# Kernel tuning notes

Hardware: AMD Instinct MI355X
Metric: run time of the kernel (lower is better)

## Reference

```python
import jax, jax.numpy as jnp
import numpy as np

B, SQ, SK, H, NH = 2, 2048, 2048, 1024, 16
HD = H // NH  # 64


def setup_inputs() -> dict:
    key = jax.random.key(0)
    ks = jax.random.split(key, 12)
    s = 1.0 / np.sqrt(H)
    inp = {
        "query": jax.random.normal(ks[0], (B, SQ, H), jnp.float32),
        "key": jax.random.normal(ks[1], (B, SK, H), jnp.float32),
        "value": jax.random.normal(ks[2], (B, SK, H), jnp.float32),
        # lower-triangular causal mask [B, SQ, SK]; nonzero = attend
        "causal_mask": jnp.broadcast_to(
            jnp.tril(jnp.ones((SQ, SK), jnp.int32)), (B, SQ, SK)
        ),
        "Wq": jax.random.uniform(ks[3], (H, H), jnp.float32, -s, s),
        "bq": jnp.zeros((H,), jnp.float32),
        "Wk": jax.random.uniform(ks[4], (H, H), jnp.float32, -s, s),
        "bk": jnp.zeros((H,), jnp.float32),
        "Wv": jax.random.uniform(ks[5], (H, H), jnp.float32, -s, s),
        "bv": jnp.zeros((H,), jnp.float32),
        "Wo": jax.random.uniform(ks[6], (H, H), jnp.float32, -s, s),
        "bo": jnp.zeros((H,), jnp.float32),
        "ln_g": jnp.ones((H,), jnp.float32),
        "ln_b": jnp.zeros((H,), jnp.float32),
    }
    return inp


def _layer_norm(x, g, b, eps=1e-5):
    mu = jnp.mean(x, axis=-1, keepdims=True)
    var = jnp.var(x, axis=-1, keepdims=True)
    return (x - mu) * jax.lax.rsqrt(var + eps) * g + b


def reference(query, key, value, causal_mask, Wq, bq, Wk, bk, Wv, bv, Wo, bo, ln_g, ln_b):
    # projections (torch Linear: x @ W.T + b)
    q = (query @ Wq.T + bq).reshape(B, SQ, NH, HD)
    k = (key @ Wk.T + bk).reshape(B, SK, NH, HD)
    v = (value @ Wv.T + bv).reshape(B, SK, NH, HD)
    # scores [B, NH, SQ, SK]
    scores = jnp.einsum("bqhd,bkhd->bhqk", q, k) / np.sqrt(HD).astype(np.float32)
    scores = jnp.where(causal_mask[:, None, :, :] == 0, -jnp.inf, scores)
    attn = jax.nn.softmax(scores, axis=-1)
    # dropout is identity in eval mode
    out = jnp.einsum("bhqk,bkhd->bqhd", attn, v).reshape(B, SQ, H)
    out = out @ Wo.T + bo
    return _layer_norm(query + out, ln_g, ln_b)
```

## Files before the change

### kernel.cpp

```cpp
#include <hip/hip_runtime.h>
#include <hip/hip_bf16.h>

#define SQL 2048
#define SKL 2048
#define HH  1024
#define NHH 16
#define HDD 64
#define BB  2
#define MM  (BB*SQL)

typedef __attribute__((ext_vector_type(8))) short short8;
typedef __attribute__((ext_vector_type(4))) short short4v;
typedef __attribute__((ext_vector_type(4))) float f32x4;
typedef unsigned short u16;

__device__ inline u16 f2bf(float f) {
    unsigned int u = __float_as_uint(f);
    u += 0x7fffu + ((u >> 16) & 1u);
    return (u16)(u >> 16);
}

__device__ inline void gl_lds16(const void* g, void* l) {
    __builtin_amdgcn_global_load_lds(
        (const __attribute__((address_space(1))) unsigned int*)g,
        (__attribute__((address_space(3))) unsigned int*)l, 16, 0, 0);
}

__global__ __launch_bounds__(256) void cvt_all_kernel(
    const float* __restrict__ q, const float* __restrict__ k, const float* __restrict__ v,
    const float* __restrict__ wq, const float* __restrict__ wk,
    const float* __restrict__ wv, const float* __restrict__ wo,
    u16* __restrict__ xq, u16* __restrict__ xk, u16* __restrict__ xv,
    u16* __restrict__ wqb, u16* __restrict__ wkb, u16* __restrict__ wvb, u16* __restrict__ wob)
{
    int b = blockIdx.x;
    const float* src; u16* dst;
    if      (b < 4096)  { src = q;  dst = xq; }
    else if (b < 8192)  { src = k;  dst = xk;  b -= 4096; }
    else if (b < 12288) { src = v;  dst = xv;  b -= 8192; }
    else if (b < 13312) { src = wq; dst = wqb; b -= 12288; }
    else if (b < 14336) { src = wk; dst = wkb; b -= 13312; }
    else if (b < 15360) { src = wv; dst = wvb; b -= 14336; }
    else                { src = wo; dst = wob; b -= 15360; }
    int i = (b * 256 + threadIdx.x) * 4;
    float4 vv = *(const float4*)(src + i);
    ushort4 oo;
    oo.x = f2bf(vv.x); oo.y = f2bf(vv.y); oo.z = f2bf(vv.z); oo.w = f2bf(vv.w);
    *(ushort4*)(dst + i) = oo;
}

__global__ __launch_bounds__(256) void proj_kernel(
    const u16* __restrict__ xq, const u16* __restrict__ xk, const u16* __restrict__ xv,
    const u16* __restrict__ wqb, const u16* __restrict__ wkb, const u16* __restrict__ wvb,
    const float* __restrict__ bq, const float* __restrict__ bk, const float* __restrict__ bv,
    u16* __restrict__ oq, u16* __restrict__ ok, u16* __restrict__ ov)
{
    const int z = blockIdx.z;
    const u16* A      = (z == 0) ? xq  : (z == 1) ? xk  : xv;
    const u16* W      = (z == 0) ? wqb : (z == 1) ? wkb : wvb;
    const float* bias = (z == 0) ? bq  : (z == 1) ? bk  : bv;
    u16* outb         = (z == 0) ? oq  : (z == 1) ? ok  : ov;
    const float scale = (z == 0) ? 0.125f * 1.4426950408889634f : 1.0f;

    __shared__ u16 lds_a[128 * 64];
    __shared__ u16 lds_b[128 * 64];

    const int t = threadIdx.x;
    const int lane = t & 63;
    const int quad = lane >> 4;
    const int lo = lane & 15;
    const int wv = t >> 6;
    const int wm = (wv >> 1) * 64, wn = (wv & 1) * 64;
    const int m0 = blockIdx.x * 128;
    const int n0 = blockIdx.y * 128;

    f32x4 acc[4][4];
#pragma unroll
    for (int i = 0; i < 4; i++)
#pragma unroll
        for (int j = 0; j < 4; j++) acc[i][j] = (f32x4){0.f, 0.f, 0.f, 0.f};

    int rr[4], cc[4];
#pragma unroll
    for (int u = 0; u < 4; u++) {
        int sl = u * 256 + t;
        rr[u] = sl >> 3;
        cc[u] = ((sl & 7) ^ (rr[u] & 7)) * 8;
    }

    for (int k0 = 0; k0 < HH; k0 += 64) {
#pragma unroll
        for (int u = 0; u < 4; u++) {
            gl_lds16(A + (size_t)(m0 + rr[u]) * HH + k0 + cc[u], &lds_a[(u * 256 + t) * 8]);
            gl_lds16(W + (size_t)(n0 + rr[u]) * HH + k0 + cc[u], &lds_b[(u * 256 + t) * 8]);
        }
        __syncthreads();
#pragma unroll
        for (int kk = 0; kk < 2; kk++) {
            short8 af[4], bf[4];
#pragma unroll
            for (int i = 0; i < 4; i++) {
                const int ra = wm + i * 16 + lo;
                const int rb = wn + i * 16 + lo;
                af[i] = *(const short8*)&lds_a[ra * 64 + (((kk * 4 + quad) ^ (ra & 7)) * 8)];
                bf[i] = *(const short8*)&lds_b[rb * 64 + (((kk * 4 + quad) ^ (rb & 7)) * 8)];
            }
            if (z == 2) {
#pragma unroll
                for (int i = 0; i < 4; i++)
#pragma unroll
                    for (int j = 0; j < 4; j++)
                        acc[i][j] = __builtin_amdgcn_mfma_f32_16x16x32_bf16(bf[j], af[i], acc[i][j], 0, 0, 0);
            } else {
#pragma unroll
                for (int i = 0; i < 4; i++)
#pragma unroll
                    for (int j = 0; j < 4; j++)
                        acc[i][j] = __builtin_amdgcn_mfma_f32_16x16x32_bf16(af[i], bf[j], acc[i][j], 0, 0, 0);
            }
        }
        __syncthreads();
    }

#pragma unroll
    for (int i = 0; i < 4; i++) {
#pragma unroll
        for (int j = 0; j < 4; j++) {
#pragma unroll
            for (int r = 0; r < 4; r++) {
                if (z == 2) {
                    int dg  = n0 + wn + j * 16 + quad * 4 + r;
                    int tok = m0 + wm + i * 16 + lo;
                    float val = acc[i][j][r] + bias[dg];
                    int head = dg >> 6, d = dg & 63;
                    int bi = tok >> 11, s = tok & 2047;
                    outb[(((size_t)bi * NHH + head) * HDD + d) * SKL + s] = f2bf(val);
                } else {
                    int row = m0 + wm + i * 16 + quad * 4 + r;
                    int col = n0 + wn + j * 16 + lo;
                    float val = (acc[i][j][r] + bias[col]) * scale;
                    int bi = row >> 11, s = row & 2047;
                    int head = col >> 6, d = col & 63;
                    outb[(((size_t)bi * NHH + head) * SQL + s) * HDD + d] = f2bf(val);
                }
            }
        }
    }
}

__global__ __launch_bounds__(256) void outproj_kernel(
    const u16* __restrict__ A, const u16* __restrict__ W,
    const float* __restrict__ bias, const float* __restrict__ resid,
    float* __restrict__ outf)
{
    __shared__ u16 lds_a[128 * 64];
    __shared__ u16 lds_b[128 * 64];

    const int t = threadIdx.x;
    const int lane = t & 63;
    const int quad = lane >> 4;
    const int lo = lane & 15;
    const int wv = t >> 6;
    const int wm = (wv >> 1) * 64, wn = (wv & 1) * 64;
    const int m0 = blockIdx.x * 128;
    const int n0 = blockIdx.y * 128;

    f32x4 acc[4][4];
#pragma unroll
    for (int i = 0; i < 4; i++)
#pragma unroll
        for (int j = 0; j < 4; j++) acc[i][j] = (f32x4){0.f, 0.f, 0.f, 0.f};

    int rr[4], cc[4];
#pragma unroll
    for (int u = 0; u < 4; u++) {
        int sl = u * 256 + t;
        rr[u] = sl >> 3;
        cc[u] = ((sl & 7) ^ (rr[u] & 7)) * 8;
    }

    for (int k0 = 0; k0 < HH; k0 += 64) {
#pragma unroll
        for (int u = 0; u < 4; u++) {
            gl_lds16(A + (size_t)(m0 + rr[u]) * HH + k0 + cc[u], &lds_a[(u * 256 + t) * 8]);
            gl_lds16(W + (size_t)(n0 + rr[u]) * HH + k0 + cc[u], &lds_b[(u * 256 + t) * 8]);
        }
        __syncthreads();
#pragma unroll
        for (int kk = 0; kk < 2; kk++) {
            short8 af[4], bf[4];
#pragma unroll
            for (int i = 0; i < 4; i++) {
                const int ra = wm + i * 16 + lo;
                const int rb = wn + i * 16 + lo;
                af[i] = *(const short8*)&lds_a[ra * 64 + (((kk * 4 + quad) ^ (ra & 7)) * 8)];
                bf[i] = *(const short8*)&lds_b[rb * 64 + (((kk * 4 + quad) ^ (rb & 7)) * 8)];
            }
#pragma unroll
            for (int i = 0; i < 4; i++)
#pragma unroll
                for (int j = 0; j < 4; j++)
                    acc[i][j] = __builtin_amdgcn_mfma_f32_16x16x32_bf16(af[i], bf[j], acc[i][j], 0, 0, 0);
        }
        __syncthreads();
    }

#pragma unroll
    for (int i = 0; i < 4; i++)
#pragma unroll
        for (int j = 0; j < 4; j++)
#pragma unroll
            for (int r = 0; r < 4; r++) {
                int row = m0 + wm + i * 16 + quad * 4 + r;
                int col = n0 + wn + j * 16 + lo;
                float val = acc[i][j][r] + bias[col] + resid[(size_t)row * HH + col];
                outf[(size_t)row * HH + col] = val;
            }
}

#define PSTR 72
#define KVB 128

__global__ __launch_bounds__(256) void attn_kernel(
    const u16* __restrict__ qb, const u16* __restrict__ kb, const u16* __restrict__ vtb,
    u16* __restrict__ attn_out)
{
    __shared__ u16 k_lds[KVB * 64];
    __shared__ u16 vt_lds[64 * KVB];
    __shared__ u16 p_lds[4 * 16 * PSTR];

    const int t = threadIdx.x;
    const int lane = t & 63;
    const int quad = lane >> 4;
    const int lo = lane & 15;
    const int w = t >> 6;
    const int qt = (SQL / 64 - 1) - (blockIdx.x >> 5);
    const int bh = blockIdx.x & 31;
    const int q0 = qt * 64;

    const u16* qbase = qb + ((size_t)bh * SQL + q0 + w * 16 + lo) * HDD + quad * 8;
    short8 qf0 = *(const short8*)qbase;
    short8 qf1 = *(const short8*)(qbase + 32);

    float m_s = -__builtin_inff(), l_s = 0.f;
    f32x4 o[4];
#pragma unroll
    for (int j = 0; j < 4; j++) o[j] = (f32x4){0.f, 0.f, 0.f, 0.f};

    int krr[4], kcc[4], vrr[4], vcc[4];
#pragma unroll
    for (int u = 0; u < 4; u++) {
        int sl = u * 256 + t;
        krr[u] = sl >> 3;  kcc[u] = ((sl & 7)  ^ (krr[u] & 7))  * 8;
        vrr[u] = sl >> 4;  vcc[u] = ((sl & 15) ^ (vrr[u] & 15)) * 8;
    }
    const u16* kbh = kb + (size_t)bh * SKL * HDD;
    const u16* vbh = vtb + (size_t)bh * HDD * SKL;
    u16* ppriv = &p_lds[w * 16 * PSTR];
    const int ql = w * 16 + lo;
    const int KT = (qt >> 1) + 1;

    for (int ti = 0; ti < KT; ti++) {
        const int k0 = ti * KVB;
#pragma unroll
        for (int u = 0; u < 4; u++) {
            gl_lds16(kbh + (size_t)(k0 + krr[u]) * HDD + kcc[u], &k_lds[(u * 256 + t) * 8]);
            gl_lds16(vbh + (size_t)vrr[u] * SKL + k0 + vcc[u], &vt_lds[(u * 256 + t) * 8]);
        }
        __syncthreads();

#pragma unroll
        for (int hb = 0; hb < 2; hb++) {
            const int kb0 = k0 + hb * 64;
            if (kb0 > q0) break;
            const bool diag = (kb0 == q0);

            f32x4 s[4];
            __builtin_amdgcn_s_setprio(1);
#pragma unroll
            for (int nt = 0; nt < 4; nt++) {
                const int row = hb * 64 + nt * 16 + lo;
                short8 kf0 = *(const short8*)&k_lds[row * 64 + ((quad ^ (row & 7)) * 8)];
                short8 kf1 = *(const short8*)&k_lds[row * 64 + (((4 + quad) ^ (row & 7)) * 8)];
                s[nt] = (f32x4){0.f, 0.f, 0.f, 0.f};
                s[nt] = __builtin_amdgcn_mfma_f32_16x16x32_bf16(kf0, qf0, s[nt], 0, 0, 0);
                s[nt] = __builtin_amdgcn_mfma_f32_16x16x32_bf16(kf1, qf1, s[nt], 0, 0, 0);
            }
            __builtin_amdgcn_s_setprio(0);
            if (diag) {
#pragma unroll
                for (int nt = 0; nt < 4; nt++)
#pragma unroll
                    for (int r = 0; r < 4; r++)
                        if (nt * 16 + quad * 4 + r > ql) s[nt][r] = -__builtin_inff();
            }

            float mx = s[0][0];
#pragma unroll
            for (int nt = 0; nt < 4; nt++)
#pragma unroll
                for (int r = 0; r < 4; r++) mx = fmaxf(mx, s[nt][r]);
            mx = fmaxf(mx, __shfl_xor(mx, 16));
            mx = fmaxf(mx, __shfl_xor(mx, 32));

            if (!__all(mx - m_s <= 8.0f)) {
                float mnew = fmaxf(m_s, mx);
                float al = __builtin_amdgcn_exp2f(m_s - mnew);
                m_s = mnew;
                l_s *= al;
                float alr[4];
#pragma unroll
                for (int r = 0; r < 4; r++) alr[r] = __shfl(al, quad * 4 + r, 16);
#pragma unroll
                for (int nt = 0; nt < 4; nt++)
#pragma unroll
                    for (int r = 0; r < 4; r++) o[nt][r] *= alr[r];
            }

            float rs = 0.f;
#pragma unroll
            for (int nt = 0; nt < 4; nt++)
#pragma unroll
                for (int r = 0; r < 4; r++) {
                    s[nt][r] = __builtin_amdgcn_exp2f(s[nt][r] - m_s);
                    rs += s[nt][r];
                }
            rs += __shfl_xor(rs, 16);
            rs += __shfl_xor(rs, 32);
            l_s += rs;

#pragma unroll
            for (int nt = 0; nt < 4; nt++) {
                short4v pk;
#pragma unroll
                for (int r = 0; r < 4; r++) pk[r] = (short)f2bf(s[nt][r]);
                *(short4v*)&ppriv[lo * PSTR + nt * 16 + quad * 4] = pk;
            }
            short8 pf0 = *(const short8*)&ppriv[lo * PSTR + quad * 8];
            short8 pf1 = *(const short8*)&ppriv[lo * PSTR + 32 + quad * 8];

            __builtin_amdgcn_s_setprio(1);
#pragma unroll
            for (int nt = 0; nt < 4; nt++) {
                const int vrow = nt * 16 + lo;
                short8 vf0 = *(const short8*)&vt_lds[vrow * KVB + (((hb * 8 + quad) ^ (vrow & 15)) * 8)];
                short8 vf1 = *(const short8*)&vt_lds[vrow * KVB + (((hb * 8 + 4 + quad) ^ (vrow & 15)) * 8)];
                o[nt] = __builtin_amdgcn_mfma_f32_16x16x32_bf16(pf0, vf0, o[nt], 0, 0, 0);
                o[nt] = __builtin_amdgcn_mfma_f32_16x16x32_bf16(pf1, vf1, o[nt], 0, 0, 0);
            }
            __builtin_amdgcn_s_setprio(0);
        }
        __syncthreads();
    }

    const int b = bh >> 4, h = bh & 15;
    float inv[4];
#pragma unroll
    for (int r = 0; r < 4; r++) inv[r] = 1.0f / __shfl(l_s, quad * 4 + r, 16);
#pragma unroll
    for (int nt = 0; nt < 4; nt++)
#pragma unroll
        for (int r = 0; r < 4; r++) {
            int srow = q0 + w * 16 + quad * 4 + r;
            attn_out[((size_t)b * SQL + srow) * HH + h * HDD + nt * 16 + lo] =
                f2bf(o[nt][r] * inv[r]);
        }
}

__global__ __launch_bounds__(256) void ln_kernel(const float* __restrict__ x,
                                                 const float* __restrict__ g,
                                                 const float* __restrict__ bb,
                                                 float* __restrict__ out)
{
    const int row = blockIdx.x;
    const int t = threadIdx.x;
    const float* xr = x + (size_t)row * HH;
    float4 v = *(const float4*)(xr + t * 4);
    float s1 = v.x + v.y + v.z + v.w;
    float s2 = v.x * v.x + v.y * v.y + v.z * v.z + v.w * v.w;
#pragma unroll
    for (int off = 32; off; off >>= 1) { s1 += __shfl_xor(s1, off); s2 += __shfl_xor(s2, off); }
    __shared__ float red[8];
    if ((t & 63) == 0) { red[(t >> 6) * 2] = s1; red[(t >> 6) * 2 + 1] = s2; }
    __syncthreads();
    s1 = red[0] + red[2] + red[4] + red[6];
    s2 = red[1] + red[3] + red[5] + red[7];
    float mu = s1 * (1.0f / HH);
    float var = s2 * (1.0f / HH) - mu * mu;
    float rstd = rsqrtf(var + 1e-5f);
    float4 gg = *(const float4*)(g + t * 4);
    float4 b4 = *(const float4*)(bb + t * 4);
    float4 o;
    o.x = (v.x - mu) * rstd * gg.x + b4.x;
    o.y = (v.y - mu) * rstd * gg.y + b4.y;
    o.z = (v.z - mu) * rstd * gg.z + b4.z;
    o.w = (v.w - mu) * rstd * gg.w + b4.w;
    *(float4*)(out + (size_t)row * HH + t * 4) = o;
}

extern "C" void kernel_launch(void* const* d_in, const int* in_sizes, int n_in,
                              void* d_out, int out_size, void* d_ws, size_t ws_size,
                              hipStream_t stream)
{
    const float* query = (const float*)d_in[0];
    const float* key   = (const float*)d_in[1];
    const float* value = (const float*)d_in[2];
    const float* Wq = (const float*)d_in[4];
    const float* bq = (const float*)d_in[5];
    const float* Wk = (const float*)d_in[6];
    const float* bk = (const float*)d_in[7];
    const float* Wv = (const float*)d_in[8];
    const float* bv = (const float*)d_in[9];
    const float* Wo = (const float*)d_in[10];
    const float* bo = (const float*)d_in[11];
    const float* ln_g = (const float*)d_in[12];
    const float* ln_b = (const float*)d_in[13];
    float* out = (float*)d_out;

    char* wp = (char*)d_ws;
    auto alloc = [&](size_t bytes) { void* p = (void*)wp; wp += (bytes + 255) & ~(size_t)255; return p; };
    const int nW = HH * HH;
    const int nX = MM * HH;
    u16* wqb = (u16*)alloc((size_t)nW * 2);
    u16* wkb = (u16*)alloc((size_t)nW * 2);
    u16* wvb = (u16*)alloc((size_t)nW * 2);
    u16* wob = (u16*)alloc((size_t)nW * 2);
    u16* xq  = (u16*)alloc((size_t)nX * 2);
    u16* xk  = (u16*)alloc((size_t)nX * 2);
    u16* xv  = (u16*)alloc((size_t)nX * 2);
    u16* qbuf = (u16*)alloc((size_t)nX * 2);
    u16* kbuf = (u16*)alloc((size_t)nX * 2);
    u16* vbuf = (u16*)alloc((size_t)nX * 2);
    u16* attnb = (u16*)alloc((size_t)nX * 2);
    float* projf = (float*)alloc((size_t)nX * 4);

    cvt_all_kernel<<<16384, 256, 0, stream>>>(query, key, value, Wq, Wk, Wv, Wo,
                                              xq, xk, xv, wqb, wkb, wvb, wob);

    proj_kernel<<<dim3(32, 8, 3), 256, 0, stream>>>(
        xq, xk, xv, wqb, wkb, wvb, bq, bk, bv, qbuf, kbuf, vbuf);

    attn_kernel<<<1024, 256, 0, stream>>>(qbuf, kbuf, vbuf, attnb);

    outproj_kernel<<<dim3(32, 8), 256, 0, stream>>>(attnb, wob, bo, query, projf);

    ln_kernel<<<MM, 256, 0, stream>>>(projf, ln_g, ln_b, out);
}
```

Before: 267.3 us.

## Process two 64-row query tiles per attention block to reuse K/V tiles

Each attention workgroup now handles 128 query rows as two 64-row sub-tiles (A and B), sharing each K/V tile load from LDS between both, and the grid is halved to 512 blocks. The aim is to halve global-to-LDS K/V traffic and barrier count per query row. The cost is doubled register use for accumulators and Q fragments, which may lower occupancy, and fewer blocks, which may hurt load balance on a causal mask. The bf16 packing of P also switches to a paired float2-to-bf16x2 conversion.

Result: slower. 284.8 us (+6.6%).

```diff
diff --git a/kernel.cpp b/kernel.cpp
--- a/kernel.cpp
+++ b/kernel.cpp
@@ -18,6 +18,13 @@
     unsigned int u = __float_as_uint(f);
     u += 0x7fffu + ((u >> 16) & 1u);
     return (u16)(u >> 16);
+}
+
+__device__ inline unsigned int bf2_bits(float a, float b) {
+    __hip_bfloat162 h = __float22bfloat162_rn(make_float2(a, b));
+    unsigned int r;
+    __builtin_memcpy(&r, &h, 4);
+    return r;
 }
 
 __device__ inline void gl_lds16(const void* g, void* l) {
@@ -234,18 +241,23 @@
     const int quad = lane >> 4;
     const int lo = lane & 15;
     const int w = t >> 6;
-    const int qt = (SQL / 64 - 1) - (blockIdx.x >> 5);
+    const int qblk = (SQL / 128 - 1) - (blockIdx.x >> 5);
     const int bh = blockIdx.x & 31;
-    const int q0 = qt * 64;
-
-    const u16* qbase = qb + ((size_t)bh * SQL + q0 + w * 16 + lo) * HDD + quad * 8;
-    short8 qf0 = *(const short8*)qbase;
-    short8 qf1 = *(const short8*)(qbase + 32);
-
-    float m_s = -__builtin_inff(), l_s = 0.f;
-    f32x4 o[4];
-#pragma unroll
-    for (int j = 0; j < 4; j++) o[j] = (f32x4){0.f, 0.f, 0.f, 0.f};
+    const int q0A = qblk * 128;
+    const int q0B = q0A + 64;
+
+    const u16* qbaseA = qb + ((size_t)bh * SQL + q0A + w * 16 + lo) * HDD + quad * 8;
+    short8 qa0 = *(const short8*)qbaseA;
+    short8 qa1 = *(const short8*)(qbaseA + 32);
+    const u16* qbaseB = qbaseA + (size_t)64 * HDD;
+    short8 qbf0 = *(const short8*)qbaseB;
+    short8 qbf1 = *(const short8*)(qbaseB + 32);
+
+    float mA = -__builtin_inff(), lA = 0.f;
+    float mB = -__builtin_inff(), lB = 0.f;
+    f32x4 oA[4], oB[4];
+#pragma unroll
+    for (int j = 0; j < 4; j++) { oA[j] = (f32x4){0.f, 0.f, 0.f, 0.f}; oB[j] = (f32x4){0.f, 0.f, 0.f, 0.f}; }
 
     int krr[4], kcc[4], vrr[4], vcc[4];
 #pragma unroll
@@ -258,8 +270,65 @@
     const u16* vbh = vtb + (size_t)bh * HDD * SKL;
     u16* ppriv = &p_lds[w * 16 * PSTR];
     const int ql = w * 16 + lo;
-    const int KT = (qt >> 1) + 1;
-
+
+    auto softmax_pv = [&](f32x4* s, float& m_s, float& l_s, f32x4* o, int hb) {
+        float mx = s[0][0];
+#pragma unroll
+        for (int nt = 0; nt < 4; nt++)
+#pragma unroll
+            for (int r = 0; r < 4; r++) mx = fmaxf(mx, s[nt][r]);
+        mx = fmaxf(mx, __shfl_xor(mx, 16));
+        mx = fmaxf(mx, __shfl_xor(mx, 32));
+
+        if (!__all(mx - m_s <= 8.0f)) {
+            float mnew = fmaxf(m_s, mx);
+            float al = __builtin_amdgcn_exp2f(m_s - mnew);
+            m_s = mnew;
+            l_s *= al;
+            float alr[4];
+#pragma unroll
+            for (int r = 0; r < 4; r++) alr[r] = __shfl(al, quad * 4 + r, 16);
+#pragma unroll
+            for (int nt = 0; nt < 4; nt++)
+#pragma unroll
+                for (int r = 0; r < 4; r++) o[nt][r] *= alr[r];
+        }
+
+        float rs = 0.f;
+#pragma unroll
+        for (int nt = 0; nt < 4; nt++)
+#pragma unroll
+            for (int r = 0; r < 4; r++) {
+                s[nt][r] = __builtin_amdgcn_exp2f(s[nt][r] - m_s);
+                rs += s[nt][r];
+            }
+        rs += __shfl_xor(rs, 16);
+        rs += __shfl_xor(rs, 32);
+        l_s += rs;
+
+#pragma unroll
+        for (int nt = 0; nt < 4; nt++) {
+            uint2 pk;
+            pk.x = bf2_bits(s[nt][0], s[nt][1]);
+            pk.y = bf2_bits(s[nt][2], s[nt][3]);
+            *(uint2*)&ppriv[lo * PSTR + nt * 16 + quad * 4] = pk;
+        }
+        short8 pf0 = *(const short8*)&ppriv[lo * PSTR + quad * 8];
+        short8 pf1 = *(const short8*)&ppriv[lo * PSTR + 32 + quad * 8];
+
+        __builtin_amdgcn_s_setprio(1);
+#pragma unroll
+        for (int nt = 0; nt < 4; nt++) {
+            const int vrow = nt * 16 + lo;
+            short8 vf0 = *(const short8*)&vt_lds[vrow * KVB + (((hb * 8 + quad) ^ (vrow & 15)) * 8)];
+            short8 vf1 = *(const short8*)&vt_lds[vrow * KVB + (((hb * 8 + 4 + quad) ^ (vrow & 15)) * 8)];
+            o[nt] = __builtin_amdgcn_mfma_f32_16x16x32_bf16(pf0, vf0, o[nt], 0, 0, 0);
+            o[nt] = __builtin_amdgcn_mfma_f32_16x16x32_bf16(pf1, vf1, o[nt], 0, 0, 0);
+        }
+        __builtin_amdgcn_s_setprio(0);
+    };
+
+    const int KT = qblk + 1;
     for (int ti = 0; ti < KT; ti++) {
         const int k0 = ti * KVB;
 #pragma unroll
@@ -272,98 +341,74 @@
 #pragma unroll
         for (int hb = 0; hb < 2; hb++) {
             const int kb0 = k0 + hb * 64;
-            if (kb0 > q0) break;
-            const bool diag = (kb0 == q0);
-
-            f32x4 s[4];
+            const bool actA = (kb0 <= q0A);
+
+            f32x4 sA[4], sB[4];
             __builtin_amdgcn_s_setprio(1);
-#pragma unroll
-            for (int nt = 0; nt < 4; nt++) {
-                const int row = hb * 64 + nt * 16 + lo;
-                short8 kf0 = *(const short8*)&k_lds[row * 64 + ((quad ^ (row & 7)) * 8)];
-                short8 kf1 = *(const short8*)&k_lds[row * 64 + (((4 + quad) ^ (row & 7)) * 8)];
-                s[nt] = (f32x4){0.f, 0.f, 0.f, 0.f};
-                s[nt] = __builtin_amdgcn_mfma_f32_16x16x32_bf16(kf0, qf0, s[nt], 0, 0, 0);
-                s[nt] = __builtin_amdgcn_mfma_f32_16x16x32_bf16(kf1, qf1, s[nt], 0, 0, 0);
+            if (actA) {
+#pragma unroll
+                for (int nt = 0; nt < 4; nt++) {
+                    const int row = hb * 64 + nt * 16 + lo;
+                    short8 kf0 = *(const short8*)&k_lds[row * 64 + ((quad ^ (row & 7)) * 8)];
+                    short8 kf1 = *(const short8*)&k_lds[row * 64 + (((4 + quad) ^ (row & 7)) * 8)];
+                    sA[nt] = (f32x4){0.f, 0.f, 0.f, 0.f};
+                    sB[nt] = (f32x4){0.f, 0.f, 0.f, 0.f};
+                    sA[nt] = __builtin_amdgcn_mfma_f32_16x16x32_bf16(kf0, qa0, sA[nt], 0, 0, 0);
+                    sA[nt] = __builtin_amdgcn_mfma_f32_16x16x32_bf16(kf1, qa1, sA[nt], 0, 0, 0);
+                    sB[nt] = __builtin_amdgcn_mfma_f32_16x16x32_bf16(kf0, qbf0, sB[nt], 0, 0, 0);
+                    sB[nt] = __builtin_amdgcn_mfma_f32_16x16x32_bf16(kf1, qbf1, sB[nt], 0, 0, 0);
+                }
+            } else {
+#pragma unroll
+                for (int nt = 0; nt < 4; nt++) {
+                    const int row = hb * 64 + nt * 16 + lo;
+                    short8 kf0 = *(const short8*)&k_lds[row * 64 + ((quad ^ (row & 7)) * 8)];
+                    short8 kf1 = *(const short8*)&k_lds[row * 64 + (((4 + quad) ^ (row & 7)) * 8)];
+                    sB[nt] = (f32x4){0.f, 0.f, 0.f, 0.f};
+                    sB[nt] = __builtin_amdgcn_mfma_f32_16x16x32_bf16(kf0, qbf0, sB[nt], 0, 0, 0);
+                    sB[nt] = __builtin_amdgcn_mfma_f32_16x16x32_bf16(kf1, qbf1, sB[nt], 0, 0, 0);
+                }
             }
             __builtin_amdgcn_s_setprio(0);
-            if (diag) {
+
+            if (actA) {
+                if (kb0 == q0A) {
+#pragma unroll
+                    for (int nt = 0; nt < 4; nt++)
+#pragma unroll
+                        for (int r = 0; r < 4; r++)
+                            if (nt * 16 + quad * 4 + r > ql) sA[nt][r] = -__builtin_inff();
+                }
+                softmax_pv(sA, mA, lA, oA, hb);
+            }
+            if (kb0 == q0B) {
 #pragma unroll
                 for (int nt = 0; nt < 4; nt++)
 #pragma unroll
                     for (int r = 0; r < 4; r++)
-                        if (nt * 16 + quad * 4 + r > ql) s[nt][r] = -__builtin_inff();
-            }
-
-            float mx = s[0][0];
-#pragma unroll
-            for (int nt = 0; nt < 4; nt++)
-#pragma unroll
-                for (int r = 0; r < 4; r++) mx = fmaxf(mx, s[nt][r]);
-            mx = fmaxf(mx, __shfl_xor(mx, 16));
-            mx = fmaxf(mx, __shfl_xor(mx, 32));
-
-            if (!__all(mx - m_s <= 8.0f)) {
-                float mnew = fmaxf(m_s, mx);
-                float al = __builtin_amdgcn_exp2f(m_s - mnew);
-                m_s = mnew;
-                l_s *= al;
-                float alr[4];
-#pragma unroll
-                for (int r = 0; r < 4; r++) alr[r] = __shfl(al, quad * 4 + r, 16);
-#pragma unroll
-                for (int nt = 0; nt < 4; nt++)
-#pragma unroll
-                    for (int r = 0; r < 4; r++) o[nt][r] *= alr[r];
-            }
-
-            float rs = 0.f;
-#pragma unroll
-            for (int nt = 0; nt < 4; nt++)
-#pragma unroll
-                for (int r = 0; r < 4; r++) {
-                    s[nt][r] = __builtin_amdgcn_exp2f(s[nt][r] - m_s);
-                    rs += s[nt][r];
-                }
-            rs += __shfl_xor(rs, 16);
-            rs += __shfl_xor(rs, 32);
-            l_s += rs;
-
-#pragma unroll
-            for (int nt = 0; nt < 4; nt++) {
-                short4v pk;
-#pragma unroll
-                for (int r = 0; r < 4; r++) pk[r] = (short)f2bf(s[nt][r]);
-                *(short4v*)&ppriv[lo * PSTR + nt * 16 + quad * 4] = pk;
-            }
-            short8 pf0 = *(const short8*)&ppriv[lo * PSTR + quad * 8];
-            short8 pf1 = *(const short8*)&ppriv[lo * PSTR + 32 + quad * 8];
-
-            __builtin_amdgcn_s_setprio(1);
-#pragma unroll
-            for (int nt = 0; nt < 4; nt++) {
-                const int vrow = nt * 16 + lo;
-                short8 vf0 = *(const short8*)&vt_lds[vrow * KVB + (((hb * 8 + quad) ^ (vrow & 15)) * 8)];
-                short8 vf1 = *(const short8*)&vt_lds[vrow * KVB + (((hb * 8 + 4 + quad) ^ (vrow & 15)) * 8)];
-                o[nt] = __builtin_amdgcn_mfma_f32_16x16x32_bf16(pf0, vf0, o[nt], 0, 0, 0);
-                o[nt] = __builtin_amdgcn_mfma_f32_16x16x32_bf16(pf1, vf1, o[nt], 0, 0, 0);
-            }
-            __builtin_amdgcn_s_setprio(0);
+                        if (nt * 16 + quad * 4 + r > ql) sB[nt][r] = -__builtin_inff();
+            }
+            softmax_pv(sB, mB, lB, oB, hb);
         }
         __syncthreads();
     }
 
     const int b = bh >> 4, h = bh & 15;
-    float inv[4];
-#pragma unroll
-    for (int r = 0; r < 4; r++) inv[r] = 1.0f / __shfl(l_s, quad * 4 + r, 16);
+    float invA[4], invB[4];
+#pragma unroll
+    for (int r = 0; r < 4; r++) {
+        invA[r] = 1.0f / __shfl(lA, quad * 4 + r, 16);
+        invB[r] = 1.0f / __shfl(lB, quad * 4 + r, 16);
+    }
 #pragma unroll
     for (int nt = 0; nt < 4; nt++)
 #pragma unroll
         for (int r = 0; r < 4; r++) {
-            int srow = q0 + w * 16 + quad * 4 + r;
-            attn_out[((size_t)b * SQL + srow) * HH + h * HDD + nt * 16 + lo] =
-                f2bf(o[nt][r] * inv[r]);
+            int srowA = q0A + w * 16 + quad * 4 + r;
+            attn_out[((size_t)b * SQL + srowA) * HH + h * HDD + nt * 16 + lo] =
+                f2bf(oA[nt][r] * invA[r]);
+            attn_out[((size_t)b * SQL + srowA + 64) * HH + h * HDD + nt * 16 + lo] =
+                f2bf(oB[nt][r] * invB[r]);
         }
 }
 
@@ -440,7 +485,7 @@
     proj_kernel<<<dim3(32, 8, 3), 256, 0, stream>>>(
         xq, xk, xv, wqb, wkb, wvb, bq, bk, bv, qbuf, kbuf, vbuf);
 
-    attn_kernel<<<1024, 256, 0, stream>>>(qbuf, kbuf, vbuf, attnb);
+    attn_kernel<<<512, 256, 0, stream>>>(qbuf, kbuf, vbuf, attnb);
 
     outproj_kernel<<<dim3(32, 8), 256, 0, stream>>>(attnb, wob, bo, query, projf);
 
```
